# Performance work log

Measured on AMD Instinct MI355X. Metric: run time of the kernel, lower is better.

## Reference

```python
import jax, jax.numpy as jnp
import numpy as np

D = 1024
H = 16
DK = D // H
FF = int(8 / 3 * D)  # 2730
EPS = 1e-6


def setup_inputs() -> dict:
    key = jax.random.key(0)
    ks = jax.random.split(key, 8)
    s = lambda n: 1.0 / np.sqrt(n)
    return {
        "x": jax.random.normal(ks[0], (2, 2048, D), dtype=jnp.float32),
        "w_qkv": jax.random.normal(ks[1], (3 * D, D), dtype=jnp.float32) * s(D),
        "w_o": jax.random.normal(ks[2], (D, D), dtype=jnp.float32) * s(D),
        "n1_w": jnp.ones((D,), dtype=jnp.float32),
        "n2_w": jnp.ones((D,), dtype=jnp.float32),
        "w1": jax.random.normal(ks[3], (FF, D), dtype=jnp.float32) * s(D),
        "w2": jax.random.normal(ks[4], (D, FF), dtype=jnp.float32) * s(FF),
        "w3": jax.random.normal(ks[5], (FF, D), dtype=jnp.float32) * s(D),
    }


def _rmsnorm(x, w):
    return x * jax.lax.rsqrt(jnp.mean(x * x, axis=-1, keepdims=True) + EPS) * w


def _attn(x, w_qkv, w_o):
    B, L, _ = x.shape
    qkv = x @ w_qkv.T                       # [B,L,3D]
    qkv = qkv.reshape(B, L, 3, H, DK)
    q, k, v = qkv[:, :, 0], qkv[:, :, 1], qkv[:, :, 2]   # [B,L,H,DK]
    scores = jnp.einsum("blhd,bmhd->bhlm", q, k) / np.sqrt(DK).astype(np.float32)
    attn = jax.nn.softmax(scores, axis=-1)               # [B,H,L,L]
    out = jnp.einsum("bhlm,bmhd->blhd", attn, v).reshape(B, L, D)
    return out @ w_o.T


def _swiglu(x, w1, w2, w3):
    return (jax.nn.silu(x @ w1.T) * (x @ w3.T)) @ w2.T


def reference(x, w_qkv, w_o, n1_w, n2_w, w1, w2, w3):
    x = x + _attn(_rmsnorm(x, n1_w), w_qkv, w_o)
    return x + _swiglu(_rmsnorm(x, n2_w), w1, w2, w3)
```

## Files before the change

kernel.cpp:

```cpp
#include <hip/hip_runtime.h>
#include <stdint.h>


#define LSEQ   2048
#define DMODEL 1024
#define NHEAD  16
#define NTOK   4096
#define FFR    2730
#define FFP    2816
#define FF2    5632

typedef short  short8  __attribute__((ext_vector_type(8)));
typedef float  floatx4 __attribute__((ext_vector_type(4)));

__device__ __forceinline__ uint16_t f2bf(float f) {
  uint32_t u = __builtin_bit_cast(uint32_t, f);
  u += 0x7FFFu + ((u >> 16) & 1u);
  return (uint16_t)(u >> 16);
}
__device__ __forceinline__ float bf2f(uint16_t s) {
  uint32_t u = ((uint32_t)s) << 16;
  return __builtin_bit_cast(float, u);
}
__device__ __forceinline__ void gl2lds16(const void* g, void* l) {
  __builtin_amdgcn_global_load_lds(
      (const __attribute__((address_space(1))) unsigned int*)g,
      (__attribute__((address_space(3))) unsigned int*)l, 16, 0, 0);
}

__global__ __launch_bounds__(256) void cvt_all_k(const float* __restrict__ wqkv,
                                                 const float* __restrict__ wo,
                                                 const float* __restrict__ w1,
                                                 const float* __restrict__ w3,
                                                 uint16_t* __restrict__ dst) {
  int g = blockIdx.x;
  int c = threadIdx.x * 4;
  const float* src = nullptr;
  if (g < 3072)       src = wqkv + (size_t)g * 1024;
  else if (g < 4096)  src = wo + (size_t)(g - 3072) * 1024;
  else if (g < 6912)  { int r = g - 4096; if (r < FFR) src = w1 + (size_t)r * 1024; }
  else                { int r = g - 6912; if (r < FFR) src = w3 + (size_t)r * 1024; }
  float4 v = src ? *(const float4*)(src + c) : float4{0, 0, 0, 0};
  uint64_t pack =  (uint64_t)f2bf(v.x)        | ((uint64_t)f2bf(v.y) << 16)
                | ((uint64_t)f2bf(v.z) << 32) | ((uint64_t)f2bf(v.w) << 48);
  *(uint64_t*)(dst + (size_t)g * 1024 + c) = pack;
}

__global__ void cvt_pad_k(const float* __restrict__ src, uint16_t* __restrict__ dst,
                          int rows, int cols, int cols_p, long total) {
  long idx = (long)blockIdx.x * 256 + threadIdx.x;
  if (idx >= total) return;
  int r = (int)(idx / cols_p);
  int c = (int)(idx % cols_p);
  float v = (r < rows && c < cols) ? src[(size_t)r * cols + c] : 0.0f;
  dst[idx] = f2bf(v);
}

__global__ __launch_bounds__(256) void rmsnorm_k(const float* __restrict__ x,
                                                 const float* __restrict__ wgt,
                                                 uint16_t* __restrict__ out) {
  const int row = blockIdx.x;
  const int c = threadIdx.x * 4;
  const float* xr = x + (size_t)row * DMODEL;
  float4 v = *(const float4*)(xr + c);
  float ss = v.x * v.x + v.y * v.y + v.z * v.z + v.w * v.w;
#pragma unroll
  for (int off = 32; off >= 1; off >>= 1) ss += __shfl_down(ss, off, 64);
  __shared__ float red[4];
  if ((threadIdx.x & 63) == 0) red[threadIdx.x >> 6] = ss;
  __syncthreads();
  float tot = red[0] + red[1] + red[2] + red[3];
  float scale = rsqrtf(tot * (1.0f / DMODEL) + 1e-6f);
  float4 wv = *(const float4*)(wgt + c);
  uint64_t pack =  (uint64_t)f2bf(v.x * scale * wv.x)
                | ((uint64_t)f2bf(v.y * scale * wv.y) << 16)
                | ((uint64_t)f2bf(v.z * scale * wv.z) << 32)
                | ((uint64_t)f2bf(v.w * scale * wv.w) << 48);
  *(uint64_t*)(out + (size_t)row * DMODEL + c) = pack;
}

__global__ __launch_bounds__(256) void silu_mul_k(const uint16_t* __restrict__ C13,
                                                  uint16_t* __restrict__ g) {
  const int row = blockIdx.y;
  const int col = (blockIdx.x * 256 + threadIdx.x) * 4;
  if (col >= FFP) return;
  const uint16_t* pa = C13 + (size_t)row * FF2 + col;
  uint64_t av = *(const uint64_t*)pa;
  uint64_t bv = *(const uint64_t*)(pa + FFP);
  uint64_t ov = 0;
#pragma unroll
  for (int e = 0; e < 4; e++) {
    float xv = bf2f((uint16_t)(av >> (16 * e)));
    float yv = bf2f((uint16_t)(bv >> (16 * e)));
    float ex = __builtin_amdgcn_exp2f(-xv * 1.4426950408889634f);
    float s = xv * __builtin_amdgcn_rcpf(1.0f + ex);
    ov |= (uint64_t)f2bf(s * yv) << (16 * e);
  }
  *(uint64_t*)(g + (size_t)row * FFP + col) = ov;
}

template <int MODE, int TM, int TN>
__global__ __launch_bounds__(256) void gemm_bt(const uint16_t* __restrict__ A,
                                               const uint16_t* __restrict__ B,
                                               uint16_t* __restrict__ Cb,
                                               float* __restrict__ Cf,
                                               const float* __restrict__ Res,
                                               int M, int N, int K) {
  constexpr int FI = TM / 32, FJ = TN / 32;
  constexpr int NIT = (TM + TN) / 64;
  __shared__ uint16_t As[TM * 32];
  __shared__ uint16_t Bs[TN * 32];
  const int tid = threadIdx.x;
  const int w = tid >> 6, lane = tid & 63;
  const int grp = lane >> 4, l16 = lane & 15;
  const int m0 = blockIdx.y * TM, n0 = blockIdx.x * TN;
  const int rw = (w >> 1) * (TM / 2), cw = (w & 1) * (TN / 2);

  floatx4 acc[FI][FJ] = {};

  const uint16_t* gp[NIT];
  uint16_t* lp[NIT];
#pragma unroll
  for (int i = 0; i < NIT; i++) {
    int c = i * 256 + tid;
    if (c < TM * 4) {
      gp[i] = A + (size_t)(m0 + (c >> 2)) * K + (c & 3) * 8;
      lp[i] = As + c * 8;
    } else {
      int c2 = c - TM * 4;
      gp[i] = B + (size_t)(n0 + (c2 >> 2)) * K + (c2 & 3) * 8;
      lp[i] = Bs + c2 * 8;
    }
  }

  for (int k0 = 0; k0 < K; k0 += 32) {
#pragma unroll
    for (int i = 0; i < NIT; i++) gl2lds16(gp[i] + k0, lp[i]);
    __syncthreads();
    short8 af[FI], bfr[FJ];
#pragma unroll
    for (int i = 0; i < FI; i++)
      af[i] = *(const short8*)(As + (rw + i * 16 + l16) * 32 + grp * 8);
#pragma unroll
    for (int j = 0; j < FJ; j++)
      bfr[j] = *(const short8*)(Bs + (cw + j * 16 + l16) * 32 + grp * 8);
#pragma unroll
    for (int i = 0; i < FI; i++)
#pragma unroll
      for (int j = 0; j < FJ; j++)
        acc[i][j] = __builtin_amdgcn_mfma_f32_16x16x32_bf16(af[i], bfr[j], acc[i][j], 0, 0, 0);
    __syncthreads();
  }

#pragma unroll
  for (int i = 0; i < FI; i++) {
#pragma unroll
    for (int j = 0; j < FJ; j++) {
      const int mrow = m0 + rw + i * 16 + grp * 4;
      const int ncol = n0 + cw + j * 16 + l16;
#pragma unroll
      for (int r = 0; r < 4; r++) {
        size_t idx = (size_t)(mrow + r) * N + ncol;
        float v = acc[i][j][r];
        if (MODE == 0) Cb[idx] = f2bf(v);
        else           Cf[idx] = v + Res[idx];
      }
    }
  }
}

__global__ __launch_bounds__(256) void attn_flash(const uint16_t* __restrict__ qkv,
                                                  uint16_t* __restrict__ outp) {
  const int tid = threadIdx.x;
  const int w = tid >> 6, lane = tid & 63;
  const int grp = lane >> 4, l16 = lane & 15;
  const int q0 = blockIdx.x * 64;
  const int h = blockIdx.y, b = blockIdx.z;

  __shared__ uint16_t Qs[512 * 8];
  __shared__ uint16_t Ks[512 * 8];
  __shared__ uint16_t Vt[64 * 76];
  __shared__ uint16_t Ps[64 * 76];

  const size_t base = ((size_t)b * LSEQ) * 3072 + (size_t)h * 64;

#pragma unroll
  for (int i = 0; i < 2; i++) {
    int c = i * 256 + tid;
    int row = c >> 3, cc = (c & 7) ^ (row & 7);
    gl2lds16(qkv + base + (size_t)(q0 + row) * 3072 + cc * 8, Qs + c * 8);
  }
  __syncthreads();

  short8 aq[2];
  const int qrow = w * 16 + l16;
#pragma unroll
  for (int kk = 0; kk < 2; kk++) {
    int cc = kk * 4 + grp;
    aq[kk] = *(const short8*)(Qs + (qrow * 8 + (cc ^ (qrow & 7))) * 8);
  }

  float lsum[4] = {0.f, 0.f, 0.f, 0.f};
  floatx4 o_acc[4] = {};
  const float C = 0.125f * 1.4426950408889634f;

  for (int kc = 0; kc < LSEQ / 64; kc++) {
    const int t0 = kc * 64;
    __syncthreads();
#pragma unroll
    for (int i = 0; i < 2; i++) {
      int c = i * 256 + tid;
      int row = c >> 3, cc = (c & 7) ^ (row & 7);
      gl2lds16(qkv + base + (size_t)(t0 + row) * 3072 + 1024 + cc * 8, Ks + c * 8);
    }
#pragma unroll
    for (int i = 0; i < 2; i++) {
      int c = i * 256 + tid;
      int tt = c & 63, db = c >> 6;
      const uint16_t* src = qkv + base + (size_t)(t0 + tt) * 3072 + 2048 + db * 8;
      uint4 vv = *(const uint4*)src;
      uint32_t uu[4] = {vv.x, vv.y, vv.z, vv.w};
#pragma unroll
      for (int e = 0; e < 4; e++) {
        Vt[(db * 8 + e * 2 + 0) * 76 + tt] = (uint16_t)(uu[e] & 0xFFFFu);
        Vt[(db * 8 + e * 2 + 1) * 76 + tt] = (uint16_t)(uu[e] >> 16);
      }
    }
    __syncthreads();

    floatx4 s_acc[4] = {};
#pragma unroll
    for (int j = 0; j < 4; j++) {
      const int krow = j * 16 + l16;
#pragma unroll
      for (int kk = 0; kk < 2; kk++) {
        int cc = kk * 4 + grp;
        short8 bk = *(const short8*)(Ks + (krow * 8 + (cc ^ (krow & 7))) * 8);
        s_acc[j] = __builtin_amdgcn_mfma_f32_16x16x32_bf16(aq[kk], bk, s_acc[j], 0, 0, 0);
      }
    }

    const int prow = w * 16 + grp * 4;
#pragma unroll
    for (int j = 0; j < 4; j++)
#pragma unroll
      for (int r = 0; r < 4; r++) {
        float pv = __builtin_amdgcn_exp2f(s_acc[j][r] * C);
        lsum[r] += pv;
        Ps[(prow + r) * 76 + j * 16 + l16] = f2bf(pv);
      }

#pragma unroll
    for (int kk = 0; kk < 2; kk++) {
      short8 ap = *(const short8*)(Ps + (w * 16 + l16) * 76 + kk * 32 + grp * 8);
#pragma unroll
      for (int jj = 0; jj < 4; jj++) {
        short8 bv = *(const short8*)(Vt + (jj * 16 + l16) * 76 + kk * 32 + grp * 8);
        o_acc[jj] = __builtin_amdgcn_mfma_f32_16x16x32_bf16(ap, bv, o_acc[jj], 0, 0, 0);
      }
    }
  }

#pragma unroll
  for (int off = 8; off >= 1; off >>= 1)
#pragma unroll
    for (int r = 0; r < 4; r++) lsum[r] += __shfl_xor(lsum[r], off, 64);
  float rinv[4];
#pragma unroll
  for (int r = 0; r < 4; r++) rinv[r] = __builtin_amdgcn_rcpf(lsum[r]);
#pragma unroll
  for (int jj = 0; jj < 4; jj++)
#pragma unroll
    for (int r = 0; r < 4; r++) {
      int row = b * LSEQ + q0 + w * 16 + grp * 4 + r;
      outp[(size_t)row * DMODEL + h * 64 + jj * 16 + l16] = f2bf(o_acc[jj][r] * rinv[r]);
    }
}

extern "C" void kernel_launch(void* const* d_in, const int* in_sizes, int n_in,
                              void* d_out, int out_size, void* d_ws, size_t ws_size,
                              hipStream_t stream) {
  const float* x    = (const float*)d_in[0];
  const float* wqkv = (const float*)d_in[1];
  const float* wo   = (const float*)d_in[2];
  const float* n1w  = (const float*)d_in[3];
  const float* n2w  = (const float*)d_in[4];
  const float* w1   = (const float*)d_in[5];
  const float* w2   = (const float*)d_in[6];
  const float* w3   = (const float*)d_in[7];
  float* out = (float*)d_out;

  char* p = (char*)d_ws;
  uint16_t* wall  = (uint16_t*)p; p += (size_t)9728 * 1024 * 2;
  uint16_t* wqkvb = wall;
  uint16_t* wob   = wall + (size_t)3072 * 1024;
  uint16_t* w13b  = wall + (size_t)4096 * 1024;
  uint16_t* w2b   = (uint16_t*)p; p += (size_t)1024 * FFP * 2;
  uint16_t* h1    = (uint16_t*)p; p += (size_t)NTOK * DMODEL * 2;
  uint16_t* qkvb  = (uint16_t*)p; p += (size_t)NTOK * 3072 * 2;
  uint16_t* attno = (uint16_t*)p; p += (size_t)NTOK * DMODEL * 2;
  float*    x1    = (float*)p;    p += (size_t)NTOK * DMODEL * 4;
  uint16_t* h2    = (uint16_t*)p; p += (size_t)NTOK * DMODEL * 2;
  uint16_t* c13   = (uint16_t*)p; p += (size_t)NTOK * FF2 * 2;
  uint16_t* gbuf  = (uint16_t*)p; p += (size_t)NTOK * FFP * 2;

  cvt_all_k<<<9728, 256, 0, stream>>>(wqkv, wo, w1, w3, wall);
  cvt_pad_k<<<(1024 * FFP) / 256, 256, 0, stream>>>(w2, w2b, 1024, FFR, FFP, 1024L * FFP);

  rmsnorm_k<<<NTOK, 256, 0, stream>>>(x, n1w, h1);
  gemm_bt<0, 128, 128><<<dim3(3072 / 128, NTOK / 128), 256, 0, stream>>>(
      h1, wqkvb, qkvb, nullptr, nullptr, NTOK, 3072, 1024);
  attn_flash<<<dim3(LSEQ / 64, NHEAD, 2), 256, 0, stream>>>(qkvb, attno);
  gemm_bt<1, 128, 64><<<dim3(1024 / 64, NTOK / 128), 256, 0, stream>>>(
      attno, wob, nullptr, x1, x, NTOK, 1024, 1024);
  rmsnorm_k<<<NTOK, 256, 0, stream>>>(x1, n2w, h2);
  gemm_bt<0, 128, 128><<<dim3(FF2 / 128, NTOK / 128), 256, 0, stream>>>(
      h2, w13b, c13, nullptr, nullptr, NTOK, FF2, 1024);
  silu_mul_k<<<dim3((FFP + 1023) / 1024, NTOK), 256, 0, stream>>>(c13, gbuf);
  gemm_bt<1, 128, 64><<<dim3(1024 / 64, NTOK / 128), 256, 0, stream>>>(
      gbuf, w2b, nullptr, out, x1, NTOK, 1024, FFP);
}
```

Baseline: 412.3 us.

## Fuse SiLU-gate into interleaved W1/W3 GEMM and restructure flash attention

Interleaves W1 and W3 rows in blocks of 32 so that each 128-wide GEMM tile holds matching gate and up columns. A new epilogue mode applies SiLU and the multiply in-register, which removes the c13 intermediate buffer and the separate silu_mul kernel. Attention now uses 128-query tiles per block, double-buffers K/V with prefetch into registers, and remaps blocks by XCD so each head/batch pair stays on one XCD for L2 locality. This trades more LDS and registers per block for less global traffic and fewer K/V reloads.

```diff
diff --git a/kernel.cpp b/kernel.cpp
--- a/kernel.cpp
+++ b/kernel.cpp
@@ -38,8 +38,12 @@
   const float* src = nullptr;
   if (g < 3072)       src = wqkv + (size_t)g * 1024;
   else if (g < 4096)  src = wo + (size_t)(g - 3072) * 1024;
-  else if (g < 6912)  { int r = g - 4096; if (r < FFR) src = w1 + (size_t)r * 1024; }
-  else                { int r = g - 6912; if (r < FFR) src = w3 + (size_t)r * 1024; }
+  else {
+    int r = g - 4096;
+    int u = r >> 6, wi = r & 63;
+    int srow = u * 32 + (wi & 31);
+    if (srow < FFR) src = ((wi < 32) ? w1 : w3) + (size_t)srow * 1024;
+  }
   float4 v = src ? *(const float4*)(src + c) : float4{0, 0, 0, 0};
   uint64_t pack =  (uint64_t)f2bf(v.x)        | ((uint64_t)f2bf(v.y) << 16)
                 | ((uint64_t)f2bf(v.z) << 32) | ((uint64_t)f2bf(v.w) << 48);
@@ -77,26 +81,6 @@
                 | ((uint64_t)f2bf(v.z * scale * wv.z) << 32)
                 | ((uint64_t)f2bf(v.w * scale * wv.w) << 48);
   *(uint64_t*)(out + (size_t)row * DMODEL + c) = pack;
-}
-
-__global__ __launch_bounds__(256) void silu_mul_k(const uint16_t* __restrict__ C13,
-                                                  uint16_t* __restrict__ g) {
-  const int row = blockIdx.y;
-  const int col = (blockIdx.x * 256 + threadIdx.x) * 4;
-  if (col >= FFP) return;
-  const uint16_t* pa = C13 + (size_t)row * FF2 + col;
-  uint64_t av = *(const uint64_t*)pa;
-  uint64_t bv = *(const uint64_t*)(pa + FFP);
-  uint64_t ov = 0;
-#pragma unroll
-  for (int e = 0; e < 4; e++) {
-    float xv = bf2f((uint16_t)(av >> (16 * e)));
-    float yv = bf2f((uint16_t)(bv >> (16 * e)));
-    float ex = __builtin_amdgcn_exp2f(-xv * 1.4426950408889634f);
-    float s = xv * __builtin_amdgcn_rcpf(1.0f + ex);
-    ov |= (uint64_t)f2bf(s * yv) << (16 * e);
-  }
-  *(uint64_t*)(g + (size_t)row * FFP + col) = ov;
 }
 
 template <int MODE, int TM, int TN>
@@ -152,18 +136,38 @@
     __syncthreads();
   }
 
-#pragma unroll
-  for (int i = 0; i < FI; i++) {
-#pragma unroll
-    for (int j = 0; j < FJ; j++) {
+  if constexpr (MODE == 2) {
+    const int half = N >> 1;
+#pragma unroll
+    for (int i = 0; i < FI; i++) {
       const int mrow = m0 + rw + i * 16 + grp * 4;
-      const int ncol = n0 + cw + j * 16 + l16;
-#pragma unroll
-      for (int r = 0; r < 4; r++) {
-        size_t idx = (size_t)(mrow + r) * N + ncol;
-        float v = acc[i][j][r];
-        if (MODE == 0) Cb[idx] = f2bf(v);
-        else           Cf[idx] = v + Res[idx];
+#pragma unroll
+      for (int j = 0; j < 2; j++) {
+        const int gcol = (n0 >> 1) + (cw >> 1) + j * 16 + l16;
+#pragma unroll
+        for (int r = 0; r < 4; r++) {
+          float a = acc[i][j][r];
+          float bv = acc[i][j + 2][r];
+          float ex = __builtin_amdgcn_exp2f(-a * 1.4426950408889634f);
+          float s = a * __builtin_amdgcn_rcpf(1.0f + ex);
+          Cb[(size_t)(mrow + r) * half + gcol] = f2bf(s * bv);
+        }
+      }
+    }
+  } else {
+#pragma unroll
+    for (int i = 0; i < FI; i++) {
+#pragma unroll
+      for (int j = 0; j < FJ; j++) {
+        const int mrow = m0 + rw + i * 16 + grp * 4;
+        const int ncol = n0 + cw + j * 16 + l16;
+#pragma unroll
+        for (int r = 0; r < 4; r++) {
+          size_t idx = (size_t)(mrow + r) * N + ncol;
+          float v = acc[i][j][r];
+          if (MODE == 0) Cb[idx] = f2bf(v);
+          else           Cf[idx] = v + Res[idx];
+        }
       }
     }
   }
@@ -174,107 +178,153 @@
   const int tid = threadIdx.x;
   const int w = tid >> 6, lane = tid & 63;
   const int grp = lane >> 4, l16 = lane & 15;
-  const int q0 = blockIdx.x * 64;
-  const int h = blockIdx.y, b = blockIdx.z;
-
-  __shared__ uint16_t Qs[512 * 8];
-  __shared__ uint16_t Ks[512 * 8];
-  __shared__ uint16_t Vt[64 * 76];
-  __shared__ uint16_t Ps[64 * 76];
+  const int lin = blockIdx.x;
+  const int xcd = lin & 7;
+  const int slot = lin >> 3;
+  const int pair = xcd * 4 + (slot >> 4);
+  const int qc = slot & 15;
+  const int h = pair & 15, b = pair >> 4;
+  const int q0 = qc * 128;
+
+  __shared__ uint16_t Qs[8192];
+  __shared__ uint16_t Ks[2][4096];
+  __shared__ uint16_t Vt[2][64 * 76];
+  __shared__ uint16_t Ps[128 * 76];
 
   const size_t base = ((size_t)b * LSEQ) * 3072 + (size_t)h * 64;
 
+#pragma unroll
+  for (int i = 0; i < 4; i++) {
+    int c = i * 256 + tid;
+    int row = c >> 3, cc = (c & 7) ^ (row & 7);
+    gl2lds16(qkv + base + (size_t)(q0 + row) * 3072 + cc * 8, Qs + c * 8);
+  }
 #pragma unroll
   for (int i = 0; i < 2; i++) {
     int c = i * 256 + tid;
     int row = c >> 3, cc = (c & 7) ^ (row & 7);
-    gl2lds16(qkv + base + (size_t)(q0 + row) * 3072 + cc * 8, Qs + c * 8);
+    gl2lds16(qkv + base + (size_t)row * 3072 + 1024 + cc * 8, Ks[0] + c * 8);
+  }
+#pragma unroll
+  for (int i = 0; i < 2; i++) {
+    int c = i * 256 + tid;
+    int tt = c & 63, db = c >> 6;
+    uint4 vv = *(const uint4*)(qkv + base + (size_t)tt * 3072 + 2048 + db * 8);
+    uint32_t uu[4] = {vv.x, vv.y, vv.z, vv.w};
+#pragma unroll
+    for (int e = 0; e < 4; e++) {
+      Vt[0][(db * 8 + e * 2 + 0) * 76 + tt] = (uint16_t)(uu[e] & 0xFFFFu);
+      Vt[0][(db * 8 + e * 2 + 1) * 76 + tt] = (uint16_t)(uu[e] >> 16);
+    }
   }
   __syncthreads();
 
-  short8 aq[2];
-  const int qrow = w * 16 + l16;
-#pragma unroll
-  for (int kk = 0; kk < 2; kk++) {
-    int cc = kk * 4 + grp;
-    aq[kk] = *(const short8*)(Qs + (qrow * 8 + (cc ^ (qrow & 7))) * 8);
-  }
-
-  float lsum[4] = {0.f, 0.f, 0.f, 0.f};
-  floatx4 o_acc[4] = {};
+  short8 aq[2][2];
+#pragma unroll
+  for (int fi = 0; fi < 2; fi++) {
+    const int qrow = w * 32 + fi * 16 + l16;
+#pragma unroll
+    for (int kk = 0; kk < 2; kk++) {
+      int cc = kk * 4 + grp;
+      aq[fi][kk] = *(const short8*)(Qs + (qrow * 8 + (cc ^ (qrow & 7))) * 8);
+    }
+  }
+
+  float lsum[2][4] = {};
+  floatx4 o_acc[2][4] = {};
   const float C = 0.125f * 1.4426950408889634f;
 
   for (int kc = 0; kc < LSEQ / 64; kc++) {
-    const int t0 = kc * 64;
-    __syncthreads();
-#pragma unroll
-    for (int i = 0; i < 2; i++) {
-      int c = i * 256 + tid;
-      int row = c >> 3, cc = (c & 7) ^ (row & 7);
-      gl2lds16(qkv + base + (size_t)(t0 + row) * 3072 + 1024 + cc * 8, Ks + c * 8);
-    }
-#pragma unroll
-    for (int i = 0; i < 2; i++) {
-      int c = i * 256 + tid;
-      int tt = c & 63, db = c >> 6;
-      const uint16_t* src = qkv + base + (size_t)(t0 + tt) * 3072 + 2048 + db * 8;
-      uint4 vv = *(const uint4*)src;
-      uint32_t uu[4] = {vv.x, vv.y, vv.z, vv.w};
-#pragma unroll
-      for (int e = 0; e < 4; e++) {
-        Vt[(db * 8 + e * 2 + 0) * 76 + tt] = (uint16_t)(uu[e] & 0xFFFFu);
-        Vt[(db * 8 + e * 2 + 1) * 76 + tt] = (uint16_t)(uu[e] >> 16);
-      }
-    }
-    __syncthreads();
-
-    floatx4 s_acc[4] = {};
+    const int cur = kc & 1, nxt = cur ^ 1;
+    const bool pre = (kc + 1 < LSEQ / 64);
+    const int t1 = (kc + 1) * 64;
+    uint4 vv[2];
+    if (pre) {
+#pragma unroll
+      for (int i = 0; i < 2; i++) {
+        int c = i * 256 + tid;
+        int row = c >> 3, cc = (c & 7) ^ (row & 7);
+        gl2lds16(qkv + base + (size_t)(t1 + row) * 3072 + 1024 + cc * 8, Ks[nxt] + c * 8);
+      }
+#pragma unroll
+      for (int i = 0; i < 2; i++) {
+        int c = i * 256 + tid;
+        int tt = c & 63, db = c >> 6;
+        vv[i] = *(const uint4*)(qkv + base + (size_t)(t1 + tt) * 3072 + 2048 + db * 8);
+      }
+    }
+
+    floatx4 s_acc[2][4] = {};
 #pragma unroll
     for (int j = 0; j < 4; j++) {
       const int krow = j * 16 + l16;
 #pragma unroll
       for (int kk = 0; kk < 2; kk++) {
         int cc = kk * 4 + grp;
-        short8 bk = *(const short8*)(Ks + (krow * 8 + (cc ^ (krow & 7))) * 8);
-        s_acc[j] = __builtin_amdgcn_mfma_f32_16x16x32_bf16(aq[kk], bk, s_acc[j], 0, 0, 0);
-      }
-    }
-
-    const int prow = w * 16 + grp * 4;
-#pragma unroll
-    for (int j = 0; j < 4; j++)
+        short8 bk = *(const short8*)(Ks[cur] + (krow * 8 + (cc ^ (krow & 7))) * 8);
+#pragma unroll
+        for (int fi = 0; fi < 2; fi++)
+          s_acc[fi][j] = __builtin_amdgcn_mfma_f32_16x16x32_bf16(aq[fi][kk], bk, s_acc[fi][j], 0, 0, 0);
+      }
+    }
+
+#pragma unroll
+    for (int fi = 0; fi < 2; fi++) {
+      const int prow = w * 32 + fi * 16 + grp * 4;
+#pragma unroll
+      for (int j = 0; j < 4; j++)
+#pragma unroll
+        for (int r = 0; r < 4; r++) {
+          float pv = __builtin_amdgcn_exp2f(s_acc[fi][j][r] * C);
+          lsum[fi][r] += pv;
+          Ps[(prow + r) * 76 + j * 16 + l16] = f2bf(pv);
+        }
+    }
+
+#pragma unroll
+    for (int kk = 0; kk < 2; kk++) {
+      short8 ap0 = *(const short8*)(Ps + (w * 32 + l16) * 76 + kk * 32 + grp * 8);
+      short8 ap1 = *(const short8*)(Ps + (w * 32 + 16 + l16) * 76 + kk * 32 + grp * 8);
+#pragma unroll
+      for (int jj = 0; jj < 4; jj++) {
+        short8 bv = *(const short8*)(Vt[cur] + (jj * 16 + l16) * 76 + kk * 32 + grp * 8);
+        o_acc[0][jj] = __builtin_amdgcn_mfma_f32_16x16x32_bf16(ap0, bv, o_acc[0][jj], 0, 0, 0);
+        o_acc[1][jj] = __builtin_amdgcn_mfma_f32_16x16x32_bf16(ap1, bv, o_acc[1][jj], 0, 0, 0);
+      }
+    }
+
+    if (pre) {
+#pragma unroll
+      for (int i = 0; i < 2; i++) {
+        int c = i * 256 + tid;
+        int tt = c & 63, db = c >> 6;
+        uint32_t uu[4] = {vv[i].x, vv[i].y, vv[i].z, vv[i].w};
+#pragma unroll
+        for (int e = 0; e < 4; e++) {
+          Vt[nxt][(db * 8 + e * 2 + 0) * 76 + tt] = (uint16_t)(uu[e] & 0xFFFFu);
+          Vt[nxt][(db * 8 + e * 2 + 1) * 76 + tt] = (uint16_t)(uu[e] >> 16);
+        }
+      }
+    }
+    __syncthreads();
+  }
+
+#pragma unroll
+  for (int off = 8; off >= 1; off >>= 1)
+#pragma unroll
+    for (int fi = 0; fi < 2; fi++)
+#pragma unroll
+      for (int r = 0; r < 4; r++) lsum[fi][r] += __shfl_xor(lsum[fi][r], off, 64);
+#pragma unroll
+  for (int fi = 0; fi < 2; fi++)
+#pragma unroll
+    for (int jj = 0; jj < 4; jj++)
 #pragma unroll
       for (int r = 0; r < 4; r++) {
-        float pv = __builtin_amdgcn_exp2f(s_acc[j][r] * C);
-        lsum[r] += pv;
-        Ps[(prow + r) * 76 + j * 16 + l16] = f2bf(pv);
-      }
-
-#pragma unroll
-    for (int kk = 0; kk < 2; kk++) {
-      short8 ap = *(const short8*)(Ps + (w * 16 + l16) * 76 + kk * 32 + grp * 8);
-#pragma unroll
-      for (int jj = 0; jj < 4; jj++) {
-        short8 bv = *(const short8*)(Vt + (jj * 16 + l16) * 76 + kk * 32 + grp * 8);
-        o_acc[jj] = __builtin_amdgcn_mfma_f32_16x16x32_bf16(ap, bv, o_acc[jj], 0, 0, 0);
-      }
-    }
-  }
-
-#pragma unroll
-  for (int off = 8; off >= 1; off >>= 1)
-#pragma unroll
-    for (int r = 0; r < 4; r++) lsum[r] += __shfl_xor(lsum[r], off, 64);
-  float rinv[4];
-#pragma unroll
-  for (int r = 0; r < 4; r++) rinv[r] = __builtin_amdgcn_rcpf(lsum[r]);
-#pragma unroll
-  for (int jj = 0; jj < 4; jj++)
-#pragma unroll
-    for (int r = 0; r < 4; r++) {
-      int row = b * LSEQ + q0 + w * 16 + grp * 4 + r;
-      outp[(size_t)row * DMODEL + h * 64 + jj * 16 + l16] = f2bf(o_acc[jj][r] * rinv[r]);
-    }
+        int row = b * LSEQ + q0 + w * 32 + fi * 16 + grp * 4 + r;
+        float o = o_acc[fi][jj][r] * __builtin_amdgcn_rcpf(lsum[fi][r]);
+        outp[(size_t)row * DMODEL + h * 64 + jj * 16 + l16] = f2bf(o);
+      }
 }
 
 extern "C" void kernel_launch(void* const* d_in, const int* in_sizes, int n_in,
@@ -301,7 +351,6 @@
   uint16_t* attno = (uint16_t*)p; p += (size_t)NTOK * DMODEL * 2;
   float*    x1    = (float*)p;    p += (size_t)NTOK * DMODEL * 4;
   uint16_t* h2    = (uint16_t*)p; p += (size_t)NTOK * DMODEL * 2;
-  uint16_t* c13   = (uint16_t*)p; p += (size_t)NTOK * FF2 * 2;
   uint16_t* gbuf  = (uint16_t*)p; p += (size_t)NTOK * FFP * 2;
 
   cvt_all_k<<<9728, 256, 0, stream>>>(wqkv, wo, w1, w3, wall);
@@ -310,13 +359,12 @@
   rmsnorm_k<<<NTOK, 256, 0, stream>>>(x, n1w, h1);
   gemm_bt<0, 128, 128><<<dim3(3072 / 128, NTOK / 128), 256, 0, stream>>>(
       h1, wqkvb, qkvb, nullptr, nullptr, NTOK, 3072, 1024);
-  attn_flash<<<dim3(LSEQ / 64, NHEAD, 2), 256, 0, stream>>>(qkvb, attno);
+  attn_flash<<<512, 256, 0, stream>>>(qkvb, attno);
   gemm_bt<1, 128, 64><<<dim3(1024 / 64, NTOK / 128), 256, 0, stream>>>(
       attno, wob, nullptr, x1, x, NTOK, 1024, 1024);
   rmsnorm_k<<<NTOK, 256, 0, stream>>>(x1, n2w, h2);
-  gemm_bt<0, 128, 128><<<dim3(FF2 / 128, NTOK / 128), 256, 0, stream>>>(
-      h2, w13b, c13, nullptr, nullptr, NTOK, FF2, 1024);
-  silu_mul_k<<<dim3((FFP + 1023) / 1024, NTOK), 256, 0, stream>>>(c13, gbuf);
+  gemm_bt<2, 128, 128><<<dim3(FF2 / 128, NTOK / 128), 256, 0, stream>>>(
+      h2, w13b, gbuf, nullptr, nullptr, NTOK, FF2, 1024);
   gemm_bt<1, 128, 64><<<dim3(1024 / 64, NTOK / 128), 256, 0, stream>>>(
       gbuf, w2b, nullptr, out, x1, NTOK, 1024, FFP);
 }
```

Result: faster. 390.7 us (-5.2%).
